# Performance work log

Hardware: AMD Instinct MI355X
Metric: run time of the kernel (lower is better)

Reference implementation:

```python
import jax, jax.numpy as jnp
import numpy as np

D_MODEL = 1024
N_HEADS = 16
D_HEAD = D_MODEL // N_HEADS
LORA_RANK = 8
LORA_ALPHA = 16
LORA_SCALING = LORA_ALPHA / LORA_RANK
NEG_INF = -1.0e9


def setup_inputs() -> dict:
    key = jax.random.key(0)
    ks = jax.random.split(key, 8)
    B, S = 2, 2048
    s_in = 1.0 / np.sqrt(D_MODEL)
    return {
        "x": jax.random.normal(ks[0], (B, S, D_MODEL), dtype=jnp.float32),
        "attention_mask": jnp.ones((B, S), dtype=jnp.int32),
        "W_qkv_kernel": jax.random.normal(ks[1], (D_MODEL, 3 * D_MODEL), jnp.float32) * s_in,
        "W_qkv_bias": jnp.zeros((3 * D_MODEL,), jnp.float32),
        "lora_A_qkv": jax.random.normal(ks[2], (D_MODEL, LORA_RANK), jnp.float32) * 0.01,
        "lora_B_qkv": jax.random.normal(ks[3], (LORA_RANK, 3 * D_MODEL), jnp.float32) * 0.01,
        "c_proj_kernel": jax.random.normal(ks[4], (D_MODEL, D_MODEL), jnp.float32) * s_in,
        "c_proj_bias": jnp.zeros((D_MODEL,), jnp.float32),
        "lora_A_proj": jax.random.normal(ks[5], (D_MODEL, LORA_RANK), jnp.float32) * 0.01,
        "lora_B_proj": jax.random.normal(ks[6], (LORA_RANK, D_MODEL), jnp.float32) * 0.01,
    }


def reference(x, attention_mask, W_qkv_kernel, W_qkv_bias, lora_A_qkv, lora_B_qkv,
              c_proj_kernel, c_proj_bias, lora_A_proj, lora_B_proj):
    B, S, _ = x.shape
    # QKV projection + LoRA adapter
    qkv = x @ W_qkv_kernel + W_qkv_bias
    qkv = qkv + ((x @ lora_A_qkv) @ lora_B_qkv) * LORA_SCALING
    q, k, v = jnp.split(qkv, 3, axis=-1)
    # [B, H, S, Dh]
    q = q.reshape(B, S, N_HEADS, D_HEAD).transpose(0, 2, 1, 3)
    k = k.reshape(B, S, N_HEADS, D_HEAD).transpose(0, 2, 1, 3)
    v = v.reshape(B, S, N_HEADS, D_HEAD).transpose(0, 2, 1, 3)
    # raw scores [B, H, S, S]
    scores = jnp.einsum("bhqd,bhkd->bhqk", q, k)
    # padding mask applied BEFORE scaling (as in the original)
    pad = (attention_mask[:, None, None, :] == 0)
    scores = jnp.where(pad, NEG_INF, scores)
    # causal mask (lower triangular kept)
    causal = jnp.tril(jnp.ones((S, S), dtype=bool))
    scores = jnp.where(causal[None, None, :, :], scores, NEG_INF)
    # scaling applied AFTER masking (faithful to source: -1e9 also divided)
    scaled = scores / jnp.sqrt(jnp.float32(D_HEAD))
    attn = jax.nn.softmax(scaled, axis=-1)
    ctx = jnp.einsum("bhqk,bhkd->bhqd", attn, v)
    ctx = ctx.transpose(0, 2, 1, 3).reshape(B, S, D_MODEL)
    out = ctx @ c_proj_kernel + c_proj_bias
    out = out + ((ctx @ lora_A_proj) @ lora_B_proj) * LORA_SCALING
    return out
```

## Files before the change

### kernel.cpp

```cpp
#include <hip/hip_runtime.h>
#include <hip/hip_bf16.h>

#define LOG2E 1.4426950408889634f
#define MASKVAL (-1.25e8f * LOG2E)

typedef __bf16 bf16x8 __attribute__((ext_vector_type(8)));
typedef __bf16 bf16x4 __attribute__((ext_vector_type(4)));
typedef short  shortx4 __attribute__((ext_vector_type(4)));
typedef float  floatx4 __attribute__((ext_vector_type(4)));

__device__ __forceinline__ floatx4 mfma16(bf16x8 a, bf16x8 b, floatx4 c) {
  return __builtin_amdgcn_mfma_f32_16x16x32_bf16(a, b, c, 0, 0, 0);
}

__device__ __forceinline__ floatx4 mfma_pv(bf16x4 a, bf16x4 b, floatx4 c) {
#if __has_builtin(__builtin_amdgcn_mfma_f32_16x16x16_bf16)
  return __builtin_amdgcn_mfma_f32_16x16x16_bf16(a, b, c, 0, 0, 0);
#else
  shortx4 as, bs;
  __builtin_memcpy(&as, &a, 8);
  __builtin_memcpy(&bs, &b, 8);
  return __builtin_amdgcn_mfma_f32_16x16x16bf16_1k(as, bs, c, 0, 0, 0);
#endif
}

__device__ __forceinline__ void load_lds16(const __bf16* g, __bf16* l) {
  __builtin_amdgcn_global_load_lds(
      (const __attribute__((address_space(1))) void*)g,
      (__attribute__((address_space(3))) void*)l, 16, 0, 0);
}

__device__ __forceinline__ float max3f(float a, float b, float c) {
  return fmaxf(a, fmaxf(b, c));
}

__global__ __launch_bounds__(256)
void fold_wt2(const float* __restrict__ Wq, const float* __restrict__ Aq,
              const float* __restrict__ Bq, __bf16* __restrict__ WTq,
              const float* __restrict__ Wp, const float* __restrict__ Ap,
              const float* __restrict__ Bp, __bf16* __restrict__ WTp) {
  __shared__ float tile[64][65];
  __shared__ float sLb[8][64];
  const int bx = blockIdx.x;
  const bool isQ = bx < 48;
  const float* W  = isQ ? Wq : Wp;
  const float* La = isQ ? Aq : Ap;
  const float* Lb = isQ ? Bq : Bp;
  __bf16* WT = isQ ? WTq : WTp;
  const int ncols = isQ ? 3072 : 1024;
  const int nt = (isQ ? bx : bx - 48) * 64;
  const int kt = blockIdx.y * 64;
  const int tid = threadIdx.x;
  const int tx = tid & 63, ty = tid >> 6;

  float rLa[8];
  *(float4*)&rLa[0] = *(const float4*)(La + (size_t)(kt + tx) * 8);
  *(float4*)&rLa[4] = *(const float4*)(La + (size_t)(kt + tx) * 8 + 4);

#pragma unroll
  for (int rep = 0; rep < 2; rep++) {
    int idx = tid + rep * 256;
    sLb[idx >> 6][idx & 63] = Lb[(size_t)(idx >> 6) * ncols + nt + (idx & 63)];
  }
#pragma unroll
  for (int rep = 0; rep < 16; rep++) {
    int i = rep * 4 + ty;
    tile[i][tx] = W[(size_t)(kt + i) * ncols + nt + tx];
  }
  __syncthreads();
#pragma unroll
  for (int rep = 0; rep < 16; rep++) {
    int i = rep * 4 + ty;
    int n = nt + i, k = kt + tx;
    float acc = tile[tx][i];
#pragma unroll
    for (int r = 0; r < 8; r++)
      acc += 2.0f * rLa[r] * sLb[r][i];
    WT[(size_t)n * 1024 + k] = (__bf16)acc;
  }
}

__global__ __launch_bounds__(256)
void cast_x(const float* __restrict__ x, __bf16* __restrict__ o) {
  int i = blockIdx.x * 256 + threadIdx.x;
  float4 v = ((const float4*)x)[i];
  bf16x4 r = {(__bf16)v.x, (__bf16)v.y, (__bf16)v.z, (__bf16)v.w};
  ((bf16x4*)o)[i] = r;
}

__global__ __launch_bounds__(256)
void gemm_qkv(const __bf16* __restrict__ WT, const __bf16* __restrict__ X,
              const float* __restrict__ bias, __bf16* __restrict__ qk,
              __bf16* __restrict__ vtb) {
  const int K = 1024;
  __shared__ alignas(16) __bf16 As[128 * 64];
  __shared__ alignas(16) __bf16 Bs[128 * 64];
  const int tid = threadIdx.x;
  const int wave = tid >> 6, lane = tid & 63;
  const int wm = wave >> 1, wn = wave & 1;
  const int quad = lane >> 4, l15 = lane & 15;
  const int p0 = blockIdx.y * 128, s0 = blockIdx.x * 128;
  const int srow8 = lane >> 3, sc8 = lane & 7;
  const int sswz = sc8 ^ srow8;

  floatx4 acc[4][4] = {};

  for (int kb = 0; kb < K; kb += 64) {
    __syncthreads();
#pragma unroll
    for (int t = 0; t < 4; t++) {
      int rbase = (wave * 4 + t) * 8;
      int row = rbase + srow8;
      load_lds16(WT + (size_t)(p0 + row) * K + kb + sswz * 8, As + rbase * 64);
      load_lds16(X + (size_t)(s0 + row) * K + kb + sswz * 8, Bs + rbase * 64);
    }
    __syncthreads();
#pragma unroll
    for (int ks = 0; ks < 2; ks++) {
      bf16x8 af[4], bfv[4];
#pragma unroll
      for (int t = 0; t < 4; t++) {
        int ra = wm * 64 + t * 16 + l15;
        int rb = wn * 64 + t * 16 + l15;
        int ch = (ks * 4 + quad) ^ (l15 & 7);
        af[t]  = *(const bf16x8*)(As + ra * 64 + ch * 8);
        bfv[t] = *(const bf16x8*)(Bs + rb * 64 + ch * 8);
      }
#pragma unroll
      for (int mi = 0; mi < 4; mi++)
#pragma unroll
        for (int ni = 0; ni < 4; ni++)
          acc[mi][ni] = mfma16(af[mi], bfv[ni], acc[mi][ni]);
    }
  }

  const float qscale = (p0 < 1024) ? 0.125f * LOG2E : 1.0f;
#pragma unroll
  for (int mi = 0; mi < 4; mi++) {
#pragma unroll
    for (int ni = 0; ni < 4; ni++) {
      int pb = p0 + wm * 64 + mi * 16 + quad * 4;
      int s  = s0 + wn * 64 + ni * 16 + l15;
      int b = s >> 11, s2 = s & 2047;
      if (p0 < 2048) {
        int part = pb >> 10, h = (pb & 1023) >> 6, dhb = pb & 63;
        bf16x4 o = {(__bf16)((acc[mi][ni][0] + bias[pb]) * qscale),
                    (__bf16)((acc[mi][ni][1] + bias[pb + 1]) * qscale),
                    (__bf16)((acc[mi][ni][2] + bias[pb + 2]) * qscale),
                    (__bf16)((acc[mi][ni][3] + bias[pb + 3]) * qscale)};
        *(bf16x4*)(qk + (size_t)part * 4194304 +
                   ((size_t)((b * 16 + h) * 2048 + s2)) * 64 + dhb) = o;
      } else {
        int h = (pb & 1023) >> 6, dhb = pb & 63;
        int off = s2 & 63, t = off >> 4, qd = (off >> 2) & 3, rr = off & 3;
        int ps2 = (s2 & ~63) | ((t >> 1) * 32 + qd * 8 + (t & 1) * 4 + rr);
#pragma unroll
        for (int r = 0; r < 4; r++)
          vtb[((size_t)((b * 16 + h) * 64 + dhb + r)) * 2048 + ps2] =
              (__bf16)(acc[mi][ni][r] + bias[pb + r]);
      }
    }
  }
}

__global__ __launch_bounds__(256)
void gemm_proj(const __bf16* __restrict__ A, const __bf16* __restrict__ BT,
               const float* __restrict__ bias, float* __restrict__ Cout, int N) {
  const int K = 1024;
  __shared__ alignas(16) __bf16 As[64 * 64];
  __shared__ alignas(16) __bf16 Bs[128 * 64];
  const int tid = threadIdx.x;
  const int wave = tid >> 6, lane = tid & 63;
  const int wm = wave >> 1, wn = wave & 1;
  const int quad = lane >> 4, l15 = lane & 15;
  const int m0 = blockIdx.y * 64, n0 = blockIdx.x * 128;
  const int srow8 = lane >> 3, sc8 = lane & 7;
  const int sswz = sc8 ^ srow8;

  floatx4 acc[2][4] = {};

  for (int kb = 0; kb < K; kb += 64) {
    __syncthreads();
#pragma unroll
    for (int t = 0; t < 2; t++) {
      int rbase = (wave * 2 + t) * 8;
      load_lds16(A + (size_t)(m0 + rbase + srow8) * K + kb + sswz * 8,
                 As + rbase * 64);
    }
#pragma unroll
    for (int t = 0; t < 4; t++) {
      int rbase = (wave * 4 + t) * 8;
      load_lds16(BT + (size_t)(n0 + rbase + srow8) * K + kb + sswz * 8,
                 Bs + rbase * 64);
    }
    __syncthreads();
#pragma unroll
    for (int ks = 0; ks < 2; ks++) {
      bf16x8 af[2], bfv[4];
      int ch = (ks * 4 + quad) ^ (l15 & 7);
#pragma unroll
      for (int t = 0; t < 2; t++)
        af[t] = *(const bf16x8*)(As + (wm * 32 + t * 16 + l15) * 64 + ch * 8);
#pragma unroll
      for (int t = 0; t < 4; t++)
        bfv[t] = *(const bf16x8*)(Bs + (wn * 64 + t * 16 + l15) * 64 + ch * 8);
#pragma unroll
      for (int mi = 0; mi < 2; mi++)
#pragma unroll
        for (int ni = 0; ni < 4; ni++)
          acc[mi][ni] = mfma16(af[mi], bfv[ni], acc[mi][ni]);
    }
  }

#pragma unroll
  for (int mi = 0; mi < 2; mi++)
#pragma unroll
    for (int ni = 0; ni < 4; ni++) {
      int n = n0 + wn * 64 + ni * 16 + l15;
#pragma unroll
      for (int r = 0; r < 4; r++) {
        int m = m0 + wm * 32 + mi * 16 + quad * 4 + r;
        Cout[(size_t)m * N + n] = acc[mi][ni][r] + bias[n];
      }
    }
}

__global__ __launch_bounds__(256)
void flash_attn(const __bf16* __restrict__ q, const __bf16* __restrict__ k,
                const __bf16* __restrict__ vt, const int* __restrict__ amask,
                __bf16* __restrict__ ctx) {
  const int S = 2048;
  __shared__ alignas(16) __bf16 Ks[2][64 * 64];
  __shared__ alignas(16) __bf16 Vs[2][64 * 64];
  const int bid = blockIdx.x;
  const int jb = 31 - (bid >> 5);
  const int bh = bid & 31;
  const int b = bh >> 4, h = bh & 15;
  const int wave = threadIdx.x >> 6, lane = threadIdx.x & 63;
  const int quad = lane >> 4, l15 = lane & 15;
  const int srow8 = lane >> 3, sc8 = lane & 7;
  const int sswz = sc8 ^ srow8;
  const int Q0 = jb * 64;
  const int qrow = Q0 + wave * 16 + l15;

  const __bf16* qp  = q  + (size_t)bh * S * 64;
  const __bf16* kp0 = k  + (size_t)bh * S * 64;
  const __bf16* vp0 = vt + (size_t)bh * 64 * S;

  int anyp = 0;
  const int npre = (jb + 4) >> 2;
  for (int it = 0; it < npre; it++) {
    int4 v = *(const int4*)(amask + b * S + it * 256 + lane * 4);
    anyp |= (v.x == 0) | (v.y == 0) | (v.z == 0) | (v.w == 0);
  }
  const bool padded = (__ballot(anyp) != 0ull);

  bf16x8 qf[2];
#pragma unroll
  for (int ks = 0; ks < 2; ks++)
    qf[ks] = *(const bf16x8*)(qp + (size_t)qrow * 64 + ks * 32 + quad * 8);

  auto STAGE = [&](int bb, int cc) {
#pragma unroll
    for (int t = 0; t < 2; t++) {
      int rbase = (wave * 2 + t) * 8;
      load_lds16(kp0 + (size_t)cc * 4096 + (size_t)(rbase + srow8) * 64 +
                     sswz * 8,
                 &Ks[bb][rbase * 64]);
    }
#pragma unroll
    for (int t = 0; t < 2; t++) {
      int rbase = (wave * 2 + t) * 8;
      load_lds16(vp0 + (size_t)(rbase + srow8) * S + cc * 64 + sswz * 8,
                 &Vs[bb][rbase * 64]);
    }
  };

  STAGE(0, 0);

  float mrun = 0.0f, lrun = 0.0f;
  floatx4 oacc[4] = {};

  for (int c = 0; c <= jb; c++) {
    const int cur = c & 1;
    if (c < jb) {
      STAGE(cur ^ 1, c + 1);
      asm volatile("s_waitcnt vmcnt(4)" ::: "memory");
    } else {
      asm volatile("s_waitcnt vmcnt(0)" ::: "memory");
    }
    __builtin_amdgcn_s_barrier();
    __builtin_amdgcn_sched_barrier(0);

    floatx4 st[4] = {};
    __builtin_amdgcn_s_setprio(1);
#pragma unroll
    for (int ks = 0; ks < 2; ks++) {
      const int ch = (ks * 4 + quad) ^ (l15 & 7);
      bf16x8 kf[4];
#pragma unroll
      for (int nt = 0; nt < 4; nt++)
        kf[nt] = *(const bf16x8*)(&Ks[cur][(nt * 16 + l15) * 64 + ch * 8]);
#pragma unroll
      for (int nt = 0; nt < 4; nt++)
        st[nt] = mfma16(kf[nt], qf[ks], st[nt]);
    }
    __builtin_amdgcn_s_setprio(0);

    if (padded) {
      int am_c = amask[b * S + c * 64 + lane];
      unsigned long long pm = __ballot(am_c == 0);
#pragma unroll
      for (int nt = 0; nt < 4; nt++) {
        int kl = nt * 16 + quad * 4;
#pragma unroll
        for (int r = 0; r < 4; r++) {
          bool pad = (pm >> (kl + r)) & 1ull;
          bool masked = pad || ((c == jb) && (kl + r > wave * 16 + l15));
          st[nt][r] = masked ? MASKVAL : st[nt][r];
        }
      }
    } else if (c == jb) {
#pragma unroll
      for (int nt = 0; nt < 4; nt++) {
        int kl = nt * 16 + quad * 4;
#pragma unroll
        for (int r = 0; r < 4; r++) {
          bool masked = kl + r > wave * 16 + l15;
          st[nt][r] = masked ? MASKVAL : st[nt][r];
        }
      }
    }

    float t0 = max3f(st[0][0], st[0][1], st[0][2]);
    float t1 = max3f(st[0][3], st[1][0], st[1][1]);
    float t2 = max3f(st[1][2], st[1][3], st[2][0]);
    float t3 = max3f(st[2][1], st[2][2], st[2][3]);
    float t4 = max3f(st[3][0], st[3][1], st[3][2]);
    float inm = fmaxf(max3f(t0, t1, t2), max3f(t3, t4, st[3][3]));
#pragma unroll
    for (int nt = 0; nt < 4; nt++)
#pragma unroll
      for (int r = 0; r < 4; r++)
        st[nt][r] = exp2f(st[nt][r] - mrun);
    float ssum = (((st[0][0] + st[0][1]) + (st[0][2] + st[0][3])) +
                  ((st[1][0] + st[1][1]) + (st[1][2] + st[1][3]))) +
                 (((st[2][0] + st[2][1]) + (st[2][2] + st[2][3])) +
                  ((st[3][0] + st[3][1]) + (st[3][2] + st[3][3])));
    if (!__all(inm - mrun <= 8.0f)) {
      float rm = fmaxf(inm, __shfl_xor(inm, 16, 64));
      rm = fmaxf(rm, __shfl_xor(rm, 32, 64));
      float mnew = fmaxf(mrun, rm);
      float al = exp2f(mrun - mnew);
      mrun = mnew;
      lrun *= al;
      ssum *= al;
#pragma unroll
      for (int nt = 0; nt < 4; nt++)
#pragma unroll
        for (int r = 0; r < 4; r++) st[nt][r] *= al;
#pragma unroll
      for (int nd = 0; nd < 4; nd++)
#pragma unroll
        for (int r = 0; r < 4; r++) oacc[nd][r] *= al;
    }
    lrun += ssum;

    bf16x4 pB[4];
#pragma unroll
    for (int nt = 0; nt < 4; nt++) {
      bf16x4 pk = {(__bf16)st[nt][0], (__bf16)st[nt][1],
                   (__bf16)st[nt][2], (__bf16)st[nt][3]};
      pB[nt] = pk;
    }

    __builtin_amdgcn_s_setprio(1);
#pragma unroll
    for (int tp = 0; tp < 2; tp++) {
      const int chv = (tp * 4 + quad) ^ (l15 & 7);
#pragma unroll
      for (int nd = 0; nd < 4; nd++) {
        bf16x8 v8 =
            *(const bf16x8*)(&Vs[cur][(nd * 16 + l15) * 64 + chv * 8]);
        bf16x4 vA0 = {v8[0], v8[1], v8[2], v8[3]};
        bf16x4 vA1 = {v8[4], v8[5], v8[6], v8[7]};
        oacc[nd] = mfma_pv(vA0, pB[2 * tp], oacc[nd]);
        oacc[nd] = mfma_pv(vA1, pB[2 * tp + 1], oacc[nd]);
      }
    }
    __builtin_amdgcn_s_setprio(0);

    __builtin_amdgcn_s_barrier();
  }

  lrun += __shfl_xor(lrun, 16, 64);
  lrun += __shfl_xor(lrun, 32, 64);

  const float linv = 1.0f / lrun;
#pragma unroll
  for (int nd = 0; nd < 4; nd++) {
    bf16x4 o = {(__bf16)(oacc[nd][0] * linv), (__bf16)(oacc[nd][1] * linv),
                (__bf16)(oacc[nd][2] * linv), (__bf16)(oacc[nd][3] * linv)};
    *(bf16x4*)(ctx + ((size_t)(b * 2048 + qrow)) * 1024 + h * 64 + nd * 16 +
               quad * 4) = o;
  }
}

extern "C" void kernel_launch(void* const* d_in, const int* in_sizes, int n_in,
                              void* d_out, int out_size, void* d_ws, size_t ws_size,
                              hipStream_t stream) {
  const float* x  = (const float*)d_in[0];
  const int*   am = (const int*)d_in[1];
  const float* Wq = (const float*)d_in[2];
  const float* bq = (const float*)d_in[3];
  const float* Aq = (const float*)d_in[4];
  const float* Bq = (const float*)d_in[5];
  const float* Wp = (const float*)d_in[6];
  const float* bp = (const float*)d_in[7];
  const float* Ap = (const float*)d_in[8];
  const float* Bp = (const float*)d_in[9];

  __bf16* wqkvT = (__bf16*)d_ws;
  __bf16* wpT   = wqkvT + (size_t)3072 * 1024;
  __bf16* xbf   = wpT   + (size_t)1024 * 1024;
  __bf16* qbuf  = xbf   + (size_t)4096 * 1024;
  __bf16* vtbuf = qbuf  + (size_t)2 * 4194304;
  __bf16* ctxb  = vtbuf + (size_t)4194304;

  fold_wt2<<<dim3(64, 16), 256, 0, stream>>>(Wq, Aq, Bq, wqkvT,
                                             Wp, Ap, Bp, wpT);
  cast_x<<<4096, 256, 0, stream>>>(x, xbf);

  gemm_qkv<<<dim3(32, 24), 256, 0, stream>>>(wqkvT, xbf, bq, qbuf, vtbuf);
  flash_attn<<<1024, 256, 0, stream>>>(qbuf, qbuf + 4194304, vtbuf, am, ctxb);
  gemm_proj<<<dim3(8, 64), 256, 0, stream>>>(ctxb, wpT, bp, (float*)d_out, 1024);
}
```

Before: 203.8 us.

## Double-buffer GEMM LDS tiles and stage QKV epilogue through shared memory

Both the QKV and projection GEMMs now use two LDS buffers, issuing the next K-tile's global-to-LDS loads before computing on the current one, with manual vmcnt waits and raw barriers. This hides global load latency behind the MFMA work. The QKV epilogue also writes results into shared memory first, then emits coalesced 16-byte stores for Q/K and for the permuted V-transpose layout, replacing scattered 2-byte stores. The costs are twice the LDS footprint, which may lower occupancy, and reliance on hand-written waitcnt counts being correct.

Result: faster. 187.2 us (-8.2%).

```diff
diff --git a/kernel.cpp b/kernel.cpp
--- a/kernel.cpp
+++ b/kernel.cpp
@@ -93,8 +93,7 @@
               const float* __restrict__ bias, __bf16* __restrict__ qk,
               __bf16* __restrict__ vtb) {
   const int K = 1024;
-  __shared__ alignas(16) __bf16 As[128 * 64];
-  __shared__ alignas(16) __bf16 Bs[128 * 64];
+  __shared__ alignas(16) __bf16 smem[32768];
   const int tid = threadIdx.x;
   const int wave = tid >> 6, lane = tid & 63;
   const int wm = wave >> 1, wn = wave & 1;
@@ -103,18 +102,33 @@
   const int srow8 = lane >> 3, sc8 = lane & 7;
   const int sswz = sc8 ^ srow8;
 
-  floatx4 acc[4][4] = {};
-
-  for (int kb = 0; kb < K; kb += 64) {
-    __syncthreads();
+  auto STAGE = [&](int bb, int kb) {
+    __bf16* Ab = smem + bb * 8192;
+    __bf16* Bb = smem + 16384 + bb * 8192;
 #pragma unroll
     for (int t = 0; t < 4; t++) {
       int rbase = (wave * 4 + t) * 8;
       int row = rbase + srow8;
-      load_lds16(WT + (size_t)(p0 + row) * K + kb + sswz * 8, As + rbase * 64);
-      load_lds16(X + (size_t)(s0 + row) * K + kb + sswz * 8, Bs + rbase * 64);
-    }
-    __syncthreads();
+      load_lds16(WT + (size_t)(p0 + row) * K + kb + sswz * 8, Ab + rbase * 64);
+      load_lds16(X + (size_t)(s0 + row) * K + kb + sswz * 8, Bb + rbase * 64);
+    }
+  };
+
+  floatx4 acc[4][4] = {};
+  STAGE(0, 0);
+
+  for (int it = 0; it < 16; it++) {
+    const int cur = it & 1;
+    if (it < 15) {
+      STAGE(cur ^ 1, (it + 1) * 64);
+      asm volatile("s_waitcnt vmcnt(8)" ::: "memory");
+    } else {
+      asm volatile("s_waitcnt vmcnt(0)" ::: "memory");
+    }
+    __builtin_amdgcn_s_barrier();
+    __builtin_amdgcn_sched_barrier(0);
+    const __bf16* Ac = smem + cur * 8192;
+    const __bf16* Bc = smem + 16384 + cur * 8192;
 #pragma unroll
     for (int ks = 0; ks < 2; ks++) {
       bf16x8 af[4], bfv[4];
@@ -123,8 +137,8 @@
         int ra = wm * 64 + t * 16 + l15;
         int rb = wn * 64 + t * 16 + l15;
         int ch = (ks * 4 + quad) ^ (l15 & 7);
-        af[t]  = *(const bf16x8*)(As + ra * 64 + ch * 8);
-        bfv[t] = *(const bf16x8*)(Bs + rb * 64 + ch * 8);
+        af[t]  = *(const bf16x8*)(Ac + ra * 64 + ch * 8);
+        bfv[t] = *(const bf16x8*)(Bc + rb * 64 + ch * 8);
       }
 #pragma unroll
       for (int mi = 0; mi < 4; mi++)
@@ -132,33 +146,67 @@
         for (int ni = 0; ni < 4; ni++)
           acc[mi][ni] = mfma16(af[mi], bfv[ni], acc[mi][ni]);
     }
-  }
-
-  const float qscale = (p0 < 1024) ? 0.125f * LOG2E : 1.0f;
-#pragma unroll
-  for (int mi = 0; mi < 4; mi++) {
-#pragma unroll
-    for (int ni = 0; ni < 4; ni++) {
-      int pb = p0 + wm * 64 + mi * 16 + quad * 4;
-      int s  = s0 + wn * 64 + ni * 16 + l15;
-      int b = s >> 11, s2 = s & 2047;
-      if (p0 < 2048) {
-        int part = pb >> 10, h = (pb & 1023) >> 6, dhb = pb & 63;
-        bf16x4 o = {(__bf16)((acc[mi][ni][0] + bias[pb]) * qscale),
-                    (__bf16)((acc[mi][ni][1] + bias[pb + 1]) * qscale),
-                    (__bf16)((acc[mi][ni][2] + bias[pb + 2]) * qscale),
-                    (__bf16)((acc[mi][ni][3] + bias[pb + 3]) * qscale)};
-        *(bf16x4*)(qk + (size_t)part * 4194304 +
-                   ((size_t)((b * 16 + h) * 2048 + s2)) * 64 + dhb) = o;
-      } else {
-        int h = (pb & 1023) >> 6, dhb = pb & 63;
-        int off = s2 & 63, t = off >> 4, qd = (off >> 2) & 3, rr = off & 3;
-        int ps2 = (s2 & ~63) | ((t >> 1) * 32 + qd * 8 + (t & 1) * 4 + rr);
-#pragma unroll
-        for (int r = 0; r < 4; r++)
-          vtb[((size_t)((b * 16 + h) * 64 + dhb + r)) * 2048 + ps2] =
-              (__bf16)(acc[mi][ni][r] + bias[pb + r]);
-      }
+    __builtin_amdgcn_s_barrier();
+  }
+
+  __bf16* ep = smem;
+  const int b = s0 >> 11, s2b = s0 & 2047;
+
+  if (p0 < 2048) {
+    const float qscale = (p0 < 1024) ? 0.125f * LOG2E : 1.0f;
+#pragma unroll
+    for (int mi = 0; mi < 4; mi++) {
+      int ch0 = wm * 64 + mi * 16 + quad * 4;
+      float4 b4 = *(const float4*)(bias + p0 + ch0);
+#pragma unroll
+      for (int ni = 0; ni < 4; ni++) {
+        int tl = wn * 64 + ni * 16 + l15;
+        bf16x4 o = {(__bf16)((acc[mi][ni][0] + b4.x) * qscale),
+                    (__bf16)((acc[mi][ni][1] + b4.y) * qscale),
+                    (__bf16)((acc[mi][ni][2] + b4.z) * qscale),
+                    (__bf16)((acc[mi][ni][3] + b4.w) * qscale)};
+        *(bf16x4*)(ep + tl * 136 + ch0) = o;
+      }
+    }
+    __syncthreads();
+    const int part = p0 >> 10;
+    const int h0 = (p0 & 1023) >> 6;
+    const int hs = wave & 1, tb = (wave >> 1) * 64;
+    __bf16* outp = qk + (size_t)part * 4194304 +
+                   ((size_t)((b * 16 + h0 + hs) * 2048 + s2b)) * 64;
+#pragma unroll
+    for (int j = 0; j < 8; j++) {
+      int tok = tb + j * 8 + (lane >> 3);
+      int dh = (lane & 7) * 8;
+      bf16x8 v = *(const bf16x8*)(ep + tok * 136 + hs * 64 + dh);
+      *(bf16x8*)(outp + (size_t)tok * 64 + dh) = v;
+    }
+  } else {
+#pragma unroll
+    for (int mi = 0; mi < 4; mi++) {
+      int ch0 = wm * 64 + mi * 16 + quad * 4;
+      float4 b4 = *(const float4*)(bias + p0 + ch0);
+#pragma unroll
+      for (int ni = 0; ni < 4; ni++) {
+        int tl = wn * 64 + ni * 16 + l15;
+        int off = tl & 63, t = off >> 4, qd = (off >> 2) & 3, rr = off & 3;
+        int ptl = (tl & 64) | ((t >> 1) * 32 + qd * 8 + (t & 1) * 4 + rr);
+        ep[(ch0 + 0) * 136 + ptl] = (__bf16)(acc[mi][ni][0] + b4.x);
+        ep[(ch0 + 1) * 136 + ptl] = (__bf16)(acc[mi][ni][1] + b4.y);
+        ep[(ch0 + 2) * 136 + ptl] = (__bf16)(acc[mi][ni][2] + b4.z);
+        ep[(ch0 + 3) * 136 + ptl] = (__bf16)(acc[mi][ni][3] + b4.w);
+      }
+    }
+    __syncthreads();
+    const int h0 = (p0 & 1023) >> 6;
+#pragma unroll
+    for (int j = 0; j < 8; j++) {
+      int ch = wave * 32 + j * 4 + (lane >> 4);
+      int to = (lane & 15) * 8;
+      bf16x8 v = *(const bf16x8*)(ep + ch * 136 + to);
+      int h = h0 + (ch >> 6), dh = ch & 63;
+      *(bf16x8*)(vtb + ((size_t)((b * 16 + h) * 64 + dh)) * 2048 + s2b + to) =
+          v;
     }
   }
 }
@@ -167,8 +215,7 @@
 void gemm_proj(const __bf16* __restrict__ A, const __bf16* __restrict__ BT,
                const float* __restrict__ bias, float* __restrict__ Cout, int N) {
   const int K = 1024;
-  __shared__ alignas(16) __bf16 As[64 * 64];
-  __shared__ alignas(16) __bf16 Bs[128 * 64];
+  __shared__ alignas(16) __bf16 smem[24576];
   const int tid = threadIdx.x;
   const int wave = tid >> 6, lane = tid & 63;
   const int wm = wave >> 1, wn = wave & 1;
@@ -177,39 +224,55 @@
   const int srow8 = lane >> 3, sc8 = lane & 7;
   const int sswz = sc8 ^ srow8;
 
-  floatx4 acc[2][4] = {};
-
-  for (int kb = 0; kb < K; kb += 64) {
-    __syncthreads();
+  auto STAGE = [&](int bb, int kb) {
+    __bf16* Ab = smem + bb * 4096;
+    __bf16* Bb = smem + 8192 + bb * 8192;
 #pragma unroll
     for (int t = 0; t < 2; t++) {
       int rbase = (wave * 2 + t) * 8;
       load_lds16(A + (size_t)(m0 + rbase + srow8) * K + kb + sswz * 8,
-                 As + rbase * 64);
+                 Ab + rbase * 64);
     }
 #pragma unroll
     for (int t = 0; t < 4; t++) {
       int rbase = (wave * 4 + t) * 8;
       load_lds16(BT + (size_t)(n0 + rbase + srow8) * K + kb + sswz * 8,
-                 Bs + rbase * 64);
-    }
-    __syncthreads();
+                 Bb + rbase * 64);
+    }
+  };
+
+  floatx4 acc[2][4] = {};
+  STAGE(0, 0);
+
+  for (int it = 0; it < 16; it++) {
+    const int cur = it & 1;
+    if (it < 15) {
+      STAGE(cur ^ 1, (it + 1) * 64);
+      asm volatile("s_waitcnt vmcnt(6)" ::: "memory");
+    } else {
+      asm volatile("s_waitcnt vmcnt(0)" ::: "memory");
+    }
+    __builtin_amdgcn_s_barrier();
+    __builtin_amdgcn_sched_barrier(0);
+    const __bf16* Ac = smem + cur * 4096;
+    const __bf16* Bc = smem + 8192 + cur * 8192;
 #pragma unroll
     for (int ks = 0; ks < 2; ks++) {
       bf16x8 af[2], bfv[4];
       int ch = (ks * 4 + quad) ^ (l15 & 7);
 #pragma unroll
       for (int t = 0; t < 2; t++)
-        af[t] = *(const bf16x8*)(As + (wm * 32 + t * 16 + l15) * 64 + ch * 8);
+        af[t] = *(const bf16x8*)(Ac + (wm * 32 + t * 16 + l15) * 64 + ch * 8);
 #pragma unroll
       for (int t = 0; t < 4; t++)
-        bfv[t] = *(const bf16x8*)(Bs + (wn * 64 + t * 16 + l15) * 64 + ch * 8);
+        bfv[t] = *(const bf16x8*)(Bc + (wn * 64 + t * 16 + l15) * 64 + ch * 8);
 #pragma unroll
       for (int mi = 0; mi < 2; mi++)
 #pragma unroll
         for (int ni = 0; ni < 4; ni++)
           acc[mi][ni] = mfma16(af[mi], bfv[ni], acc[mi][ni]);
     }
+    __builtin_amdgcn_s_barrier();
   }
 
 #pragma unroll
```
